# Optimization experiments

Measured on AMD Instinct MI355X. Metric: run time of the kernel, lower is better.

Reference implementation:

```python
import jax, jax.numpy as jnp
import numpy as np

EPS = 1e-6
B, S, D = 2, 2048, 2048
NH, NKV, HD = 16, 4, 128
DFF = 5632
WINDOW = 512


def rmsnorm(x, w):
    var = jnp.mean(x * x, axis=-1, keepdims=True)
    return x * jax.lax.rsqrt(var + EPS) * w


def rotate_half(x):
    x1, x2 = jnp.split(x, 2, axis=-1)
    return jnp.concatenate([-x2, x1], axis=-1)


def apply_rope(x, cos, sin):
    # x: (B, H, S, HD); cos/sin: (S, HD)
    return x * cos[None, None] + rotate_half(x) * sin[None, None]


def setup_inputs() -> dict:
    key = jax.random.key(0)
    ks = jax.random.split(key, 12)
    s = lambda n: (1.0 / np.sqrt(n))
    inp = {
        "hidden_states": jax.random.normal(ks[0], (B, S, D), jnp.float32),
        "cos": jnp.cos(jnp.arange(S)[:, None] / (10000.0 ** (jnp.concatenate([jnp.arange(HD // 2), jnp.arange(HD // 2)]) * 2.0 / HD))),
        "sin": jnp.sin(jnp.arange(S)[:, None] / (10000.0 ** (jnp.concatenate([jnp.arange(HD // 2), jnp.arange(HD // 2)]) * 2.0 / HD))),
        "ln1_w": jnp.ones((D,), jnp.float32),
        "ln2_w": jnp.ones((D,), jnp.float32),
        "wq": jax.random.normal(ks[1], (NH * HD, D), jnp.float32) * s(D),
        "wk": jax.random.normal(ks[2], (NKV * HD, D), jnp.float32) * s(D),
        "wv": jax.random.normal(ks[3], (NKV * HD, D), jnp.float32) * s(D),
        "wo": jax.random.normal(ks[4], (D, NH * HD), jnp.float32) * s(NH * HD),
        "w_gate": jax.random.normal(ks[5], (DFF, D), jnp.float32) * s(D),
        "w_up": jax.random.normal(ks[6], (DFF, D), jnp.float32) * s(D),
        "w_down": jax.random.normal(ks[7], (D, DFF), jnp.float32) * s(DFF),
    }
    return inp


def reference(hidden_states, cos, sin, ln1_w, ln2_w, wq, wk, wv, wo, w_gate, w_up, w_down):
    x = hidden_states
    # --- attention block ---
    h = rmsnorm(x, ln1_w)
    q = jnp.einsum("bsd,ed->bse", h, wq).reshape(B, S, NH, HD).transpose(0, 2, 1, 3)
    k = jnp.einsum("bsd,ed->bse", h, wk).reshape(B, S, NKV, HD).transpose(0, 2, 1, 3)
    v = jnp.einsum("bsd,ed->bse", h, wv).reshape(B, S, NKV, HD).transpose(0, 2, 1, 3)
    q = apply_rope(q, cos, sin)
    k = apply_rope(k, cos, sin)
    rep = NH // NKV
    k = jnp.repeat(k, rep, axis=1)  # (B, NH, S, HD)
    v = jnp.repeat(v, rep, axis=1)
    scale = 1.0 / np.sqrt(HD)
    scores = jnp.einsum("bhqd,bhkd->bhqk", q, k) * scale
    pos = jnp.arange(S)
    diff = pos[:, None] - pos[None, :]
    allowed = (diff >= 0) & (diff < WINDOW)  # causal + sliding window
    scores = jnp.where(allowed[None, None], scores, jnp.finfo(scores.dtype).min)
    attn = jax.nn.softmax(scores, axis=-1)
    out = jnp.einsum("bhqk,bhkd->bhqd", attn, v)
    out = out.transpose(0, 2, 1, 3).reshape(B, S, NH * HD)
    out = jnp.einsum("bse,de->bsd", out, wo)
    x = x + out
    # --- SwiGLU MLP block ---
    h = rmsnorm(x, ln2_w)
    gate = jax.nn.silu(jnp.einsum("bsd,fd->bsf", h, w_gate))
    up = jnp.einsum("bsd,fd->bsf", h, w_up)
    mlp = jnp.einsum("bsf,df->bsd", gate * up, w_down)
    return x + mlp
```

## Files before the change

kernel.cpp:

```cpp
#include <hip/hip_runtime.h>

typedef unsigned short u16;
typedef __attribute__((ext_vector_type(8))) short bf16x8;
typedef __attribute__((ext_vector_type(8))) unsigned short u16x8;
typedef __attribute__((ext_vector_type(4))) float f32x4;
typedef __attribute__((ext_vector_type(4))) _Float16 f16x4;

__device__ __forceinline__ u16 f2bf(float f) {
  union { float f; unsigned u; } v; v.f = f;
  unsigned r = v.u + 0x7fffu + ((v.u >> 16) & 1u);
  return (u16)(r >> 16);
}
__device__ __forceinline__ float bf2f(u16 u) {
  union { unsigned u; float f; } v; v.u = ((unsigned)u) << 16; return v.f;
}

#define GLOBAL_LOAD_LDS16(g, l)                                                \
  __builtin_amdgcn_global_load_lds(                                            \
      (const __attribute__((address_space(1))) void*)(g),                      \
      (__attribute__((address_space(3))) void*)(l), 16, 0, 0)

#define PHASE_SYNC()                                                            \
  __builtin_amdgcn_s_barrier();                                                 \
  asm volatile("s_waitcnt lgkmcnt(0)" ::: "memory");                            \
  __builtin_amdgcn_sched_barrier(0)

__global__ __launch_bounds__(256) void rmsnorm_k(const float* __restrict__ x,
                                                 const float* __restrict__ w,
                                                 u16* __restrict__ out) {
  __shared__ float red[4];
  const int t = threadIdx.x;
  const size_t base = (size_t)blockIdx.x * 2048 + t * 8;
  float4 a = *(const float4*)(x + base);
  float4 b = *(const float4*)(x + base + 4);
  float ss = a.x * a.x + a.y * a.y + a.z * a.z + a.w * a.w +
             b.x * b.x + b.y * b.y + b.z * b.z + b.w * b.w;
#pragma unroll
  for (int o = 32; o; o >>= 1) ss += __shfl_xor(ss, o);
  if ((t & 63) == 0) red[t >> 6] = ss;
  __syncthreads();
  float rs = rsqrtf((red[0] + red[1] + red[2] + red[3]) * (1.0f / 2048.0f) + 1e-6f);
  float4 wa = *(const float4*)(w + t * 8);
  float4 wb = *(const float4*)(w + t * 8 + 4);
  u16x8 o8;
  o8[0] = f2bf(a.x * rs * wa.x); o8[1] = f2bf(a.y * rs * wa.y);
  o8[2] = f2bf(a.z * rs * wa.z); o8[3] = f2bf(a.w * rs * wa.w);
  o8[4] = f2bf(b.x * rs * wb.x); o8[5] = f2bf(b.y * rs * wb.y);
  o8[6] = f2bf(b.z * rs * wb.z); o8[7] = f2bf(b.w * rs * wb.w);
  *(u16x8*)(out + base) = o8;
}

__global__ __launch_bounds__(256) void rope_k(u16* __restrict__ buf,
                                              const float* __restrict__ cosp,
                                              const float* __restrict__ sinp,
                                              int nh, int total) {
  int i = blockIdx.x * 256 + threadIdx.x;
  if (i >= total) return;
  int d = i & 63;
  int hh = (i >> 6) % nh;
  int row = i / (64 * nh);
  int s = row & 2047;
  u16* p = buf + (size_t)row * (nh * 128) + hh * 128 + d;
  float x1 = bf2f(p[0]), x2 = bf2f(p[64]);
  float c1 = cosp[s * 128 + d], s1 = sinp[s * 128 + d];
  float c2 = cosp[s * 128 + d + 64], s2 = sinp[s * 128 + d + 64];
  p[0]  = f2bf(x1 * c1 - x2 * s1);
  p[64] = f2bf(x2 * c2 + x1 * s2);
}

__global__ __launch_bounds__(256) void rope_qkv(u16* __restrict__ buf,
                                                const float* __restrict__ cosp,
                                                const float* __restrict__ sinp) {
  int i = blockIdx.x * 256 + threadIdx.x;
  int d = i & 63;
  int hh = (i >> 6) % 20;
  int row = i / 1280;
  int s = row & 2047;
  int col = (hh < 16) ? hh * 128 + d : 2048 + (hh - 16) * 128 + d;
  u16* p = buf + (size_t)row * 3072 + col;
  float x1 = bf2f(p[0]), x2 = bf2f(p[64]);
  float c1 = cosp[s * 128 + d], s1 = sinp[s * 128 + d];
  float c2 = cosp[s * 128 + d + 64], s2 = sinp[s * 128 + d + 64];
  p[0]  = f2bf(x1 * c1 - x2 * s1);
  p[64] = f2bf(x2 * c2 + x1 * s2);
}

__global__ __launch_bounds__(256) void cvt_k(const float* __restrict__ s,
                                             u16* __restrict__ d, int n) {
  int stride = gridDim.x * 256 * 8;
  for (int i = (blockIdx.x * 256 + threadIdx.x) * 8; i < n; i += stride) {
    float4 a = *(const float4*)(s + i);
    float4 b = *(const float4*)(s + i + 4);
    u16x8 o;
    o[0] = f2bf(a.x); o[1] = f2bf(a.y); o[2] = f2bf(a.z); o[3] = f2bf(a.w);
    o[4] = f2bf(b.x); o[5] = f2bf(b.y); o[6] = f2bf(b.z); o[7] = f2bf(b.w);
    *(u16x8*)(d + i) = o;
  }
}

__global__ __launch_bounds__(256) void cvt3_k(const float* __restrict__ s0,
                                              const float* __restrict__ s1,
                                              const float* __restrict__ s2,
                                              u16* __restrict__ d,
                                              int n0, int n1, int n2) {
  int total = n0 + n1 + n2;
  int stride = gridDim.x * 256 * 8;
  for (int i = (blockIdx.x * 256 + threadIdx.x) * 8; i < total; i += stride) {
    const float* s; int off;
    if (i < n0)            { s = s0; off = i; }
    else if (i < n0 + n1)  { s = s1; off = i - n0; }
    else                   { s = s2; off = i - n0 - n1; }
    float4 a = *(const float4*)(s + off);
    float4 b = *(const float4*)(s + off + 4);
    u16x8 o;
    o[0] = f2bf(a.x); o[1] = f2bf(a.y); o[2] = f2bf(a.z); o[3] = f2bf(a.w);
    o[4] = f2bf(b.x); o[5] = f2bf(b.y); o[6] = f2bf(b.z); o[7] = f2bf(b.w);
    *(u16x8*)(d + i) = o;
  }
}

__device__ __forceinline__ void tile_swz(int bid, int nwg, int tm, int& bm, int& bn) {
  int cpx = nwg >> 3;
  int w = (bid & 7) * cpx + (bid >> 3);
  bm = w % tm;
  bn = w / tm;
}

template <int EPI>
__global__ __launch_bounds__(512, 2) void gemm4p(const u16* __restrict__ A,
                                                 const u16* __restrict__ Bw,
                                                 void* Cout, const float* resid,
                                                 int M, int N, int K) {
  const int NK = K >> 6;
  __shared__ u16 lds[49152];
  const int t = threadIdx.x, lane = t & 63, w = t >> 6;
  const int wm = w >> 2, wn = w & 3;
  const int l15 = lane & 15, lg = lane >> 4;
  int bm, bn;
  tile_swz(blockIdx.x, gridDim.x, M >> 8, bm, bn);

  const int r64 = t >> 3;
  const int gsrc = ((t & 7) ^ (r64 & 7)) * 8;
  const u16* Asrc[4];
#pragma unroll
  for (int u = 0; u < 4; ++u)
    Asrc[u] = A + (size_t)(bm * 256 + u * 64 + r64) * K + gsrc;
  const u16* Bsrc[2];
#pragma unroll
  for (int u = 0; u < 2; ++u)
    Bsrc[u] = Bw + (size_t)(bn * 128 + u * 64 + r64) * K + gsrc;
  const int d0 = t * 8;

#define STG_A4(buf, u, kt)                                                     \
  GLOBAL_LOAD_LDS16(Asrc[u] + (kt) * 64, &lds[(buf) * 24576 + (u) * 4096 + d0])
#define STG_B4(buf, u, kt)                                                     \
  GLOBAL_LOAD_LDS16(Bsrc[u] + (kt) * 64,                                       \
                    &lds[(buf) * 24576 + 16384 + (u) * 4096 + d0])

  const int swz0 = (lg ^ (l15 & 7)) * 8;
  const int swz1 = ((4 + lg) ^ (l15 & 7)) * 8;
  const int abase = (wm * 128 + l15) * 64;
  const int bbase = 16384 + (wn * 32 + l15) * 64;

  f32x4 acc[8][2] = {};
  bf16x8 af[4], bf0[2], bf1[2];

  STG_A4(0, 0, 0); STG_A4(0, 1, 0); STG_A4(0, 2, 0); STG_A4(0, 3, 0);
  STG_B4(0, 0, 0); STG_B4(0, 1, 0);
  STG_B4(1, 0, 1); STG_B4(1, 1, 1);
  asm volatile("s_waitcnt vmcnt(2)" ::: "memory");
  __builtin_amdgcn_s_barrier();

  for (int T = 0; T < NK; ++T) {
    const int bb = (T & 1) * 24576;
    const int nbuf = (T + 1) & 1, cbuf = T & 1;
#pragma unroll
    for (int i = 0; i < 4; ++i)
      af[i] = *(const bf16x8*)&lds[bb + abase + i * 1024 + swz0];
#pragma unroll
    for (int n = 0; n < 2; ++n)
      bf0[n] = *(const bf16x8*)&lds[bb + bbase + n * 1024 + swz0];
    if (T < NK - 1) { STG_A4(nbuf, 0, T + 1); STG_A4(nbuf, 1, T + 1); }
    PHASE_SYNC();
    __builtin_amdgcn_s_setprio(1);
#pragma unroll
    for (int i = 0; i < 4; ++i)
#pragma unroll
      for (int n = 0; n < 2; ++n)
        acc[i][n] = __builtin_amdgcn_mfma_f32_16x16x32_bf16(af[i], bf0[n], acc[i][n], 0, 0, 0);
    __builtin_amdgcn_s_setprio(0);
    __builtin_amdgcn_s_barrier();
#pragma unroll
    for (int i = 0; i < 4; ++i)
      af[i] = *(const bf16x8*)&lds[bb + abase + i * 1024 + swz1];
#pragma unroll
    for (int n = 0; n < 2; ++n)
      bf1[n] = *(const bf16x8*)&lds[bb + bbase + n * 1024 + swz1];
    if (T < NK - 1) { STG_A4(nbuf, 2, T + 1); STG_A4(nbuf, 3, T + 1); }
    PHASE_SYNC();
    __builtin_amdgcn_s_setprio(1);
#pragma unroll
    for (int i = 0; i < 4; ++i)
#pragma unroll
      for (int n = 0; n < 2; ++n)
        acc[i][n] = __builtin_amdgcn_mfma_f32_16x16x32_bf16(af[i], bf1[n], acc[i][n], 0, 0, 0);
    __builtin_amdgcn_s_setprio(0);
    __builtin_amdgcn_s_barrier();
#pragma unroll
    for (int i = 0; i < 4; ++i)
      af[i] = *(const bf16x8*)&lds[bb + abase + (4 + i) * 1024 + swz0];
    if (T < NK - 2) STG_B4(cbuf, 0, T + 2);
    PHASE_SYNC();
    __builtin_amdgcn_s_setprio(1);
#pragma unroll
    for (int i = 0; i < 4; ++i)
#pragma unroll
      for (int n = 0; n < 2; ++n)
        acc[4 + i][n] = __builtin_amdgcn_mfma_f32_16x16x32_bf16(af[i], bf0[n], acc[4 + i][n], 0, 0, 0);
    __builtin_amdgcn_s_setprio(0);
    __builtin_amdgcn_s_barrier();
#pragma unroll
    for (int i = 0; i < 4; ++i)
      af[i] = *(const bf16x8*)&lds[bb + abase + (4 + i) * 1024 + swz1];
    if (T < NK - 2) STG_B4(cbuf, 1, T + 2);
    PHASE_SYNC();
    __builtin_amdgcn_s_setprio(1);
#pragma unroll
    for (int i = 0; i < 4; ++i)
#pragma unroll
      for (int n = 0; n < 2; ++n)
        acc[4 + i][n] = __builtin_amdgcn_mfma_f32_16x16x32_bf16(af[i], bf1[n], acc[4 + i][n], 0, 0, 0);
    __builtin_amdgcn_s_setprio(0);
    if (T < NK - 2) asm volatile("s_waitcnt vmcnt(2)" ::: "memory");
    else            asm volatile("s_waitcnt vmcnt(0)" ::: "memory");
    __builtin_amdgcn_s_barrier();
  }
#undef STG_A4
#undef STG_B4

#pragma unroll
  for (int mf = 0; mf < 8; ++mf)
#pragma unroll
    for (int nf = 0; nf < 2; ++nf)
#pragma unroll
      for (int r = 0; r < 4; ++r) {
        int row = bm * 256 + wm * 128 + mf * 16 + lg * 4 + r;
        int col = bn * 128 + wn * 32 + nf * 16 + l15;
        size_t idx = (size_t)row * N + col;
        if (EPI == 0)
          ((u16*)Cout)[idx] = f2bf(acc[mf][nf][r]);
        else
          ((float*)Cout)[idx] = resid[idx] + acc[mf][nf][r];
      }
}

__global__ __launch_bounds__(512, 2) void gu256(const u16* __restrict__ A,
                                                const u16* __restrict__ Wg,
                                                const u16* __restrict__ Wu,
                                                u16* __restrict__ G) {
  constexpr int KD = 2048, NK = 32;
  __shared__ u16 lds[65536];
  const int t = threadIdx.x, lane = t & 63, w = t >> 6;
  const int wm = w >> 2, wn = w & 3;
  const int l15 = lane & 15, lg = lane >> 4;
  int bm, bn;
  tile_swz(blockIdx.x, gridDim.x, 16, bm, bn);

  const int l8 = lane >> 3, g8 = lane & 7;
  const int gsrc = (g8 ^ l8) * 8;
  const u16* Asrc[2][2];
#pragma unroll
  for (int ha = 0; ha < 2; ++ha)
#pragma unroll
    for (int c = 0; c < 2; ++c)
      Asrc[ha][c] = A + (size_t)(bm * 256 + ha * 128 + w * 16 + c * 8 + l8) * KD + gsrc;
  const u16* Wsel = ((w >> 1) & 1) ? Wu : Wg;
  const u16* Bsrc[2][2];
#pragma unroll
  for (int hb = 0; hb < 2; ++hb)
#pragma unroll
    for (int c = 0; c < 2; ++c)
      Bsrc[hb][c] = Wsel + (size_t)(bn * 128 + (hb * 2 + (w >> 2)) * 32 +
                                    (w & 1) * 16 + c * 8 + l8) * KD + gsrc;
  const int dst_wl = w * 1024 + lane * 8;

#define STG_A(buf, ha, kt) do {                                                \
    GLOBAL_LOAD_LDS16(Asrc[ha][0] + (kt) * 64,                                 \
                      &lds[(buf) * 32768 + (ha) * 8192 + dst_wl]);             \
    GLOBAL_LOAD_LDS16(Asrc[ha][1] + (kt) * 64,                                 \
                      &lds[(buf) * 32768 + (ha) * 8192 + dst_wl + 512]); } while (0)
#define STG_B(buf, hb, kt) do {                                                \
    GLOBAL_LOAD_LDS16(Bsrc[hb][0] + (kt) * 64,                                 \
                      &lds[(buf) * 32768 + 16384 + (hb) * 8192 + dst_wl]);     \
    GLOBAL_LOAD_LDS16(Bsrc[hb][1] + (kt) * 64,                                 \
                      &lds[(buf) * 32768 + 16384 + (hb) * 8192 + dst_wl + 512]); } while (0)

  const int swz0 = (lg ^ (l15 & 7)) * 8;
  const int swz1 = ((4 + lg) ^ (l15 & 7)) * 8;
  const int abase = (wm * 128 + l15) * 64;
  const int bbase = 16384 + (wn * 64 + l15) * 64;

  f32x4 acc[8][4] = {};
  bf16x8 af[4], bf0[4], bf1[4];

  STG_A(0, 0, 0); STG_A(0, 1, 0);
  STG_B(0, 0, 0); STG_B(0, 1, 0);
  STG_B(1, 0, 1); STG_B(1, 1, 1);
  asm volatile("s_waitcnt vmcnt(4)" ::: "memory");
  __builtin_amdgcn_s_barrier();

  for (int T = 0; T < NK; ++T) {
    const int bb = (T & 1) * 32768;
    const int nbuf = (T + 1) & 1, cbuf = T & 1;
#pragma unroll
    for (int i = 0; i < 4; ++i)
      af[i] = *(const bf16x8*)&lds[bb + abase + i * 1024 + swz0];
#pragma unroll
    for (int n = 0; n < 4; ++n)
      bf0[n] = *(const bf16x8*)&lds[bb + bbase + n * 1024 + swz0];
    if (T < NK - 1) STG_A(nbuf, 0, T + 1);
    PHASE_SYNC();
    __builtin_amdgcn_s_setprio(1);
#pragma unroll
    for (int i = 0; i < 4; ++i)
#pragma unroll
      for (int n = 0; n < 4; ++n)
        acc[i][n] = __builtin_amdgcn_mfma_f32_16x16x32_bf16(af[i], bf0[n], acc[i][n], 0, 0, 0);
    __builtin_amdgcn_s_setprio(0);
    __builtin_amdgcn_s_barrier();
#pragma unroll
    for (int i = 0; i < 4; ++i)
      af[i] = *(const bf16x8*)&lds[bb + abase + i * 1024 + swz1];
#pragma unroll
    for (int n = 0; n < 4; ++n)
      bf1[n] = *(const bf16x8*)&lds[bb + bbase + n * 1024 + swz1];
    if (T < NK - 1) STG_A(nbuf, 1, T + 1);
    PHASE_SYNC();
    __builtin_amdgcn_s_setprio(1);
#pragma unroll
    for (int i = 0; i < 4; ++i)
#pragma unroll
      for (int n = 0; n < 4; ++n)
        acc[i][n] = __builtin_amdgcn_mfma_f32_16x16x32_bf16(af[i], bf1[n], acc[i][n], 0, 0, 0);
    __builtin_amdgcn_s_setprio(0);
    __builtin_amdgcn_s_barrier();
#pragma unroll
    for (int i = 0; i < 4; ++i)
      af[i] = *(const bf16x8*)&lds[bb + abase + (4 + i) * 1024 + swz0];
    if (T < NK - 2) STG_B(cbuf, 0, T + 2);
    PHASE_SYNC();
    __builtin_amdgcn_s_setprio(1);
#pragma unroll
    for (int i = 0; i < 4; ++i)
#pragma unroll
      for (int n = 0; n < 4; ++n)
        acc[4 + i][n] = __builtin_amdgcn_mfma_f32_16x16x32_bf16(af[i], bf0[n], acc[4 + i][n], 0, 0, 0);
    __builtin_amdgcn_s_setprio(0);
    __builtin_amdgcn_s_barrier();
#pragma unroll
    for (int i = 0; i < 4; ++i)
      af[i] = *(const bf16x8*)&lds[bb + abase + (4 + i) * 1024 + swz1];
    if (T < NK - 2) STG_B(cbuf, 1, T + 2);
    PHASE_SYNC();
    __builtin_amdgcn_s_setprio(1);
#pragma unroll
    for (int i = 0; i < 4; ++i)
#pragma unroll
      for (int n = 0; n < 4; ++n)
        acc[4 + i][n] = __builtin_amdgcn_mfma_f32_16x16x32_bf16(af[i], bf1[n], acc[4 + i][n], 0, 0, 0);
    __builtin_amdgcn_s_setprio(0);
    if (T < NK - 2) asm volatile("s_waitcnt vmcnt(4)" ::: "memory");
    else            asm volatile("s_waitcnt vmcnt(0)" ::: "memory");
    __builtin_amdgcn_s_barrier();
  }
#undef STG_A
#undef STG_B

  const size_t grow0 = (size_t)(bm * 256 + wm * 128 + lg * 4);
  const int gcol0 = bn * 128 + wn * 32 + l15;
#pragma unroll
  for (int mf = 0; mf < 8; ++mf)
#pragma unroll
    for (int p = 0; p < 2; ++p)
#pragma unroll
      for (int r = 0; r < 4; ++r) {
        float gg = acc[mf][p][r], uu = acc[mf][p + 2][r];
        float sg = gg / (1.0f + __expf(-gg));
        G[(grow0 + mf * 16 + r) * 5632 + gcol0 + p * 16] = f2bf(sg * uu);
      }
}

template <int EPI>
__global__ __launch_bounds__(256) void gemm_bt(const u16* __restrict__ A,
                                               const float* __restrict__ Bw,
                                               void* Cout, const float* resid,
                                               int M, int N, int K) {
  __shared__ u16 sA[128 * 32];
  __shared__ u16 sB[128 * 40];
  const int t = threadIdx.x, lane = t & 63, w = t >> 6;
  const int l15 = lane & 15, lg = lane >> 4;
  const int tn = N >> 7;
  const int bm = blockIdx.x / tn, bn = blockIdx.x % tn;
  const int wr = (w >> 1) << 6, wc = (w & 1) << 6;

  const u16* Ag  = A + (size_t)(bm * 128 + (t >> 2)) * K + (t & 3) * 8;
  const u16* Ag2 = Ag + (size_t)64 * K;
  const float* Bg  = Bw + (size_t)(bn * 128 + (t >> 2)) * K + (t & 3) * 8;
  const float* Bg2 = Bg + (size_t)64 * K;
  u16* sBp  = &sB[(t >> 2) * 40 + (t & 3) * 8];
  u16* sBp2 = sBp + 64 * 40;

  f32x4 acc[4][4] = {};

  for (int kt = 0; kt < K; kt += 32) {
    float4 b0 = *(const float4*)(Bg + kt);
    float4 b1 = *(const float4*)(Bg + kt + 4);
    float4 c0 = *(const float4*)(Bg2 + kt);
    float4 c1 = *(const float4*)(Bg2 + kt + 4);
    GLOBAL_LOAD_LDS16(Ag + kt, &sA[t * 8]);
    GLOBAL_LOAD_LDS16(Ag2 + kt, &sA[64 * 32 + t * 8]);
    u16x8 bs;
    bs[0] = f2bf(b0.x); bs[1] = f2bf(b0.y); bs[2] = f2bf(b0.z); bs[3] = f2bf(b0.w);
    bs[4] = f2bf(b1.x); bs[5] = f2bf(b1.y); bs[6] = f2bf(b1.z); bs[7] = f2bf(b1.w);
    *(u16x8*)sBp = bs;
    bs[0] = f2bf(c0.x); bs[1] = f2bf(c0.y); bs[2] = f2bf(c0.z); bs[3] = f2bf(c0.w);
    bs[4] = f2bf(c1.x); bs[5] = f2bf(c1.y); bs[6] = f2bf(c1.z); bs[7] = f2bf(c1.w);
    *(u16x8*)sBp2 = bs;
    __syncthreads();
    bf16x8 af[4], bfr[4];
#pragma unroll
    for (int m = 0; m < 4; ++m)
      af[m] = *(const bf16x8*)&sA[(wr + m * 16 + l15) * 32 + lg * 8];
#pragma unroll
    for (int n = 0; n < 4; ++n)
      bfr[n] = *(const bf16x8*)&sB[(wc + n * 16 + l15) * 40 + lg * 8];
#pragma unroll
    for (int m = 0; m < 4; ++m)
#pragma unroll
      for (int n = 0; n < 4; ++n)
        acc[m][n] = __builtin_amdgcn_mfma_f32_16x16x32_bf16(af[m], bfr[n], acc[m][n], 0, 0, 0);
    __syncthreads();
  }
#pragma unroll
  for (int m = 0; m < 4; ++m)
#pragma unroll
    for (int n = 0; n < 4; ++n)
#pragma unroll
      for (int r = 0; r < 4; ++r) {
        int row = bm * 128 + wr + m * 16 + lg * 4 + r;
        int col = bn * 128 + wc + n * 16 + l15;
        size_t idx = (size_t)row * N + col;
        if (EPI == 0)
          ((u16*)Cout)[idx] = f2bf(acc[m][n][r]);
        else
          ((float*)Cout)[idx] = resid[idx] + acc[m][n][r];
      }
}

__global__ __launch_bounds__(512) void gemm_gateup(const u16* __restrict__ A,
                                                   const float* __restrict__ Wg,
                                                   const float* __restrict__ Wu,
                                                   u16* __restrict__ G) {
  constexpr int N = 5632, K = 2048;
  __shared__ u16 sA[128 * 32];
  __shared__ u16 sB1[128 * 40];
  __shared__ u16 sB2[128 * 40];
  const int t = threadIdx.x, lane = t & 63, w = t >> 6;
  const int l15 = lane & 15, lg = lane >> 4;
  const int bm = blockIdx.x / 44, bn = blockIdx.x % 44;
  const int wr = (w >> 2) << 6, wc = (w & 3) << 5;

  const u16* Ag = A + (size_t)(bm * 128 + (t >> 2)) * K + (t & 3) * 8;
  const float* Bg1 = Wg + (size_t)(bn * 128 + (t >> 2)) * K + (t & 3) * 8;
  const float* Bg2 = Wu + (size_t)(bn * 128 + (t >> 2)) * K + (t & 3) * 8;
  const int sboff = (t >> 2) * 40 + (t & 3) * 8;

  f32x4 acc1[4][2] = {};
  f32x4 acc2[4][2] = {};

  for (int kt = 0; kt < K; kt += 32) {
    float4 g0 = *(const float4*)(Bg1 + kt);
    float4 g1 = *(const float4*)(Bg1 + kt + 4);
    float4 u0 = *(const float4*)(Bg2 + kt);
    float4 u1 = *(const float4*)(Bg2 + kt + 4);
    GLOBAL_LOAD_LDS16(Ag + kt, &sA[t * 8]);
    u16x8 bs;
    bs[0] = f2bf(g0.x); bs[1] = f2bf(g0.y); bs[2] = f2bf(g0.z); bs[3] = f2bf(g0.w);
    bs[4] = f2bf(g1.x); bs[5] = f2bf(g1.y); bs[6] = f2bf(g1.z); bs[7] = f2bf(g1.w);
    *(u16x8*)&sB1[sboff] = bs;
    bs[0] = f2bf(u0.x); bs[1] = f2bf(u0.y); bs[2] = f2bf(u0.z); bs[3] = f2bf(u0.w);
    bs[4] = f2bf(u1.x); bs[5] = f2bf(u1.y); bs[6] = f2bf(u1.z); bs[7] = f2bf(u1.w);
    *(u16x8*)&sB2[sboff] = bs;
    __syncthreads();
    bf16x8 af[4], b1f[2], b2f[2];
#pragma unroll
    for (int m = 0; m < 4; ++m)
      af[m] = *(const bf16x8*)&sA[(wr + m * 16 + l15) * 32 + lg * 8];
#pragma unroll
    for (int n = 0; n < 2; ++n) {
      b1f[n] = *(const bf16x8*)&sB1[(wc + n * 16 + l15) * 40 + lg * 8];
      b2f[n] = *(const bf16x8*)&sB2[(wc + n * 16 + l15) * 40 + lg * 8];
    }
#pragma unroll
    for (int m = 0; m < 4; ++m)
#pragma unroll
      for (int n = 0; n < 2; ++n) {
        acc1[m][n] = __builtin_amdgcn_mfma_f32_16x16x32_bf16(af[m], b1f[n], acc1[m][n], 0, 0, 0);
        acc2[m][n] = __builtin_amdgcn_mfma_f32_16x16x32_bf16(af[m], b2f[n], acc2[m][n], 0, 0, 0);
      }
    __syncthreads();
  }
#pragma unroll
  for (int m = 0; m < 4; ++m)
#pragma unroll
    for (int n = 0; n < 2; ++n)
#pragma unroll
      for (int r = 0; r < 4; ++r) {
        int row = bm * 128 + wr + m * 16 + lg * 4 + r;
        int col = bn * 128 + wc + n * 16 + l15;
        float ga = acc1[m][n][r], uu = acc2[m][n][r];
        float sg = ga / (1.0f + __expf(-ga));
        G[(size_t)row * N + col] = f2bf(sg * uu);
      }
}

__global__ __launch_bounds__(256) void attn_k(const u16* __restrict__ Q,
                                              const u16* __restrict__ K,
                                              const u16* __restrict__ V,
                                              u16* __restrict__ O,
                                              int qstr, int kvstr) {
  const int lane = threadIdx.x & 63;
  const int wid = blockIdx.x * 4 + (threadIdx.x >> 6);
  const int qt = wid & 127;
  const int h = (wid >> 7) & 15;
  const int b = wid >> 11;
  const int q0 = qt << 4;
  const int kvh = h >> 2;
  const int l15 = lane & 15, lg = lane >> 4;

  bf16x8 qf[4];
  {
    const u16* qp = Q + (size_t)((b << 11) + q0 + l15) * qstr + h * 128 + lg * 8;
#pragma unroll
    for (int ds = 0; ds < 4; ++ds) qf[ds] = *(const bf16x8*)(qp + ds * 32);
  }
  float m_run = -1e30f, l_run = 0.0f;
  f32x4 oacc[8];
#pragma unroll
  for (int db = 0; db < 8; ++db) oacc[db] = f32x4{0.f, 0.f, 0.f, 0.f};

  int lo = q0 - 511;
  if (lo < 0) lo = 0;
  for (int kb = (lo & ~15); kb <= q0; kb += 16) {
    f32x4 st = {0.f, 0.f, 0.f, 0.f};
    const u16* kp = K + (size_t)((b << 11) + kb + l15) * kvstr + kvh * 128 + lg * 8;
#pragma unroll
    for (int ds = 0; ds < 4; ++ds)
      st = __builtin_amdgcn_mfma_f32_16x16x32_bf16(*(const bf16x8*)(kp + ds * 32),
                                                   qf[ds], st, 0, 0, 0);
    const int qpos = q0 + l15;
    float pe[4];
    float tmax = -1e30f;
#pragma unroll
    for (int r = 0; r < 4; ++r) {
      int j = kb + lg * 4 + r;
      int d = qpos - j;
      bool ok = (d >= 0) && (d < 512);
      pe[r] = ok ? st[r] * 0.08838834764831845f : -1e30f;
      tmax = fmaxf(tmax, pe[r]);
    }
    tmax = fmaxf(tmax, __shfl_xor(tmax, 16));
    tmax = fmaxf(tmax, __shfl_xor(tmax, 32));
    float m_new = fmaxf(m_run, tmax);
    float corr = __expf(m_run - m_new);
    float psum = 0.0f;
#pragma unroll
    for (int r = 0; r < 4; ++r) {
      float e = (pe[r] > -1e29f) ? __expf(pe[r] - m_new) : 0.0f;
      pe[r] = e;
      psum += e;
    }
    psum += __shfl_xor(psum, 16);
    psum += __shfl_xor(psum, 32);
    l_run = l_run * corr + psum;
    m_run = m_new;

    f16x4 pf;
#pragma unroll
    for (int r = 0; r < 4; ++r) pf[r] = (_Float16)pe[r];

    float f0 = __shfl(corr, lg * 4 + 0);
    float f1 = __shfl(corr, lg * 4 + 1);
    float f2 = __shfl(corr, lg * 4 + 2);
    float f3 = __shfl(corr, lg * 4 + 3);
    const u16* vp = V + (size_t)((b << 11) + kb + lg * 4) * kvstr + kvh * 128 + l15;
#pragma unroll
    for (int db = 0; db < 8; ++db) {
      oacc[db][0] *= f0; oacc[db][1] *= f1; oacc[db][2] *= f2; oacc[db][3] *= f3;
      f16x4 vf;
#pragma unroll
      for (int e = 0; e < 4; ++e)
        vf[e] = (_Float16)bf2f(vp[(size_t)e * kvstr + db * 16]);
      oacc[db] = __builtin_amdgcn_mfma_f32_16x16x16f16(pf, vf, oacc[db], 0, 0, 0);
    }
  }
  float inv = 1.0f / l_run;
  float g0 = __shfl(inv, lg * 4 + 0);
  float g1 = __shfl(inv, lg * 4 + 1);
  float g2 = __shfl(inv, lg * 4 + 2);
  float g3 = __shfl(inv, lg * 4 + 3);
  u16* op = O + (size_t)((b << 11) + q0 + lg * 4) * 2048 + h * 128 + l15;
#pragma unroll
  for (int db = 0; db < 8; ++db) {
    op[0 * 2048 + db * 16] = f2bf(oacc[db][0] * g0);
    op[1 * 2048 + db * 16] = f2bf(oacc[db][1] * g1);
    op[2 * 2048 + db * 16] = f2bf(oacc[db][2] * g2);
    op[3 * 2048 + db * 16] = f2bf(oacc[db][3] * g3);
  }
}

extern "C" void kernel_launch(void* const* d_in, const int* in_sizes, int n_in,
                              void* d_out, int out_size, void* d_ws, size_t ws_size,
                              hipStream_t stream) {
  const float* x    = (const float*)d_in[0];
  const float* cosp = (const float*)d_in[1];
  const float* sinp = (const float*)d_in[2];
  const float* ln1  = (const float*)d_in[3];
  const float* ln2  = (const float*)d_in[4];
  const float* wq   = (const float*)d_in[5];
  const float* wk   = (const float*)d_in[6];
  const float* wv   = (const float*)d_in[7];
  const float* wo   = (const float*)d_in[8];
  const float* wg   = (const float*)d_in[9];
  const float* wu   = (const float*)d_in[10];
  const float* wd   = (const float*)d_in[11];
  float* out = (float*)d_out;

  const size_t SZ_HQ  = 8388608;
  const size_t SZ_KV  = 2097152;
  const size_t SZ_QKV = 12582912;
  const size_t SZ_G   = 23068672;
  const size_t SZ_WB  = 23068672;
  const size_t need_old = (SZ_HQ * 3 + SZ_KV * 2 + SZ_G) * 2;
  const size_t need_new = (SZ_HQ * 2 + SZ_QKV + SZ_G + SZ_WB) * 2;
  if (ws_size < need_old) return;

  if (ws_size >= need_new) {
    u16* h   = (u16*)d_ws;
    u16* qkv = h + SZ_HQ;
    u16* at  = qkv + SZ_QKV;
    u16* g   = at + SZ_HQ;
    u16* wb  = g + SZ_G;
    u16* wqb = wb;
    u16* wob = wb;
    u16* wgb = wb;
    u16* wdb = wb;

    rmsnorm_k<<<4096, 256, 0, stream>>>(x, ln1, h);
    cvt3_k<<<2048, 256, 0, stream>>>(wq, wk, wv, wqb, 4194304, 1048576, 1048576);
    gemm4p<0><<<384, 512, 0, stream>>>(h, wqb, qkv, nullptr, 4096, 3072, 2048);
    rope_qkv<<<20480, 256, 0, stream>>>(qkv, cosp, sinp);
    attn_k<<<1024, 256, 0, stream>>>(qkv, qkv + 2048, qkv + 2560, at, 3072, 3072);
    cvt_k<<<2048, 256, 0, stream>>>(wo, wob, 4194304);
    gemm4p<1><<<256, 512, 0, stream>>>(at, wob, d_out, x, 4096, 2048, 2048);
    rmsnorm_k<<<4096, 256, 0, stream>>>(out, ln2, h);
    cvt3_k<<<2048, 256, 0, stream>>>(wg, wu, wu, wgb, 11534336, 11534336, 0);
    gu256<<<704, 512, 0, stream>>>(h, wgb, wgb + 11534336, g);
    cvt_k<<<2048, 256, 0, stream>>>(wd, wdb, 11534336);
    gemm4p<1><<<256, 512, 0, stream>>>(g, wdb, d_out, out, 4096, 2048, 5632);
  } else {
    u16* h  = (u16*)d_ws;
    u16* q  = h + SZ_HQ;
    u16* kk = q + SZ_HQ;
    u16* vv = kk + SZ_KV;
    u16* at = vv + SZ_KV;
    u16* g  = at + SZ_HQ;

    rmsnorm_k<<<4096, 256, 0, stream>>>(x, ln1, h);
    gemm_bt<0><<<512, 256, 0, stream>>>(h, wq, q,  nullptr, 4096, 2048, 2048);
    gemm_bt<0><<<128, 256, 0, stream>>>(h, wk, kk, nullptr, 4096, 512, 2048);
    gemm_bt<0><<<128, 256, 0, stream>>>(h, wv, vv, nullptr, 4096, 512, 2048);
    rope_k<<<16384, 256, 0, stream>>>(q, cosp, sinp, 16, 4194304);
    rope_k<<<4096, 256, 0, stream>>>(kk, cosp, sinp, 4, 1048576);
    attn_k<<<1024, 256, 0, stream>>>(q, kk, vv, at, 2048, 512);
    gemm_bt<1><<<512, 256, 0, stream>>>(at, wo, d_out, x, 4096, 2048, 2048);
    rmsnorm_k<<<4096, 256, 0, stream>>>(out, ln2, h);
    gemm_gateup<<<1408, 512, 0, stream>>>(h, wg, wu, g);
    gemm_bt<1><<<512, 256, 0, stream>>>(g, wd, d_out, out, 4096, 2048, 5632);
  }
}
```

Before: 602.8 us.

## Rework GEMM to 128x256 tiles with triple-buffered LDS and fewer barriers

Replaces the 256x128 double-buffered four-phase GEMM with a 128x256 tile kernel that uses a three-stage LDS ring, prefetches two k-tiles ahead and needs one workgroup barrier per k-tile instead of four. The intra-phase barriers are also dropped from the shared phase macro, which affects the gate/up kernel as well. The goal is less barrier stall and deeper load/compute overlap. The cost is more LDS per block (about 147 KB), and the gate/up kernel may now have a write-after-read race on its current buffer without the mid-iteration barriers.

```diff
diff --git a/kernel.cpp b/kernel.cpp
--- a/kernel.cpp
+++ b/kernel.cpp
@@ -20,10 +20,10 @@
       (const __attribute__((address_space(1))) void*)(g),                      \
       (__attribute__((address_space(3))) void*)(l), 16, 0, 0)
 
-#define PHASE_SYNC()                                                            \
-  __builtin_amdgcn_s_barrier();                                                 \
-  asm volatile("s_waitcnt lgkmcnt(0)" ::: "memory");                            \
-  __builtin_amdgcn_sched_barrier(0)
+#define PHASE_TAIL()                                                           \
+  asm volatile("s_waitcnt lgkmcnt(0)" ::: "memory");                           \
+  __builtin_amdgcn_sched_barrier(0);                                           \
+  __builtin_amdgcn_s_setprio(1)
 
 __global__ __launch_bounds__(256) void rmsnorm_k(const float* __restrict__ x,
                                                  const float* __restrict__ w,
@@ -127,125 +127,99 @@
 }
 
 template <int EPI>
-__global__ __launch_bounds__(512, 2) void gemm4p(const u16* __restrict__ A,
+__global__ __launch_bounds__(512, 2) void gemm2p(const u16* __restrict__ A,
                                                  const u16* __restrict__ Bw,
                                                  void* Cout, const float* resid,
                                                  int M, int N, int K) {
   const int NK = K >> 6;
-  __shared__ u16 lds[49152];
+  __shared__ u16 lds[73728];
   const int t = threadIdx.x, lane = t & 63, w = t >> 6;
   const int wm = w >> 2, wn = w & 3;
   const int l15 = lane & 15, lg = lane >> 4;
   int bm, bn;
-  tile_swz(blockIdx.x, gridDim.x, M >> 8, bm, bn);
+  tile_swz(blockIdx.x, gridDim.x, M >> 7, bm, bn);
 
   const int r64 = t >> 3;
   const int gsrc = ((t & 7) ^ (r64 & 7)) * 8;
-  const u16* Asrc[4];
+  const u16* Asrc[2];
+#pragma unroll
+  for (int u = 0; u < 2; ++u)
+    Asrc[u] = A + (size_t)(bm * 128 + u * 64 + r64) * K + gsrc;
+  const u16* Bsrc[4];
 #pragma unroll
   for (int u = 0; u < 4; ++u)
-    Asrc[u] = A + (size_t)(bm * 256 + u * 64 + r64) * K + gsrc;
-  const u16* Bsrc[2];
-#pragma unroll
-  for (int u = 0; u < 2; ++u)
-    Bsrc[u] = Bw + (size_t)(bn * 128 + u * 64 + r64) * K + gsrc;
+    Bsrc[u] = Bw + (size_t)(bn * 256 + u * 64 + r64) * K + gsrc;
   const int d0 = t * 8;
 
-#define STG_A4(buf, u, kt)                                                     \
+#define STG_A2(buf, u, kt)                                                     \
   GLOBAL_LOAD_LDS16(Asrc[u] + (kt) * 64, &lds[(buf) * 24576 + (u) * 4096 + d0])
-#define STG_B4(buf, u, kt)                                                     \
+#define STG_B2(buf, u, kt)                                                     \
   GLOBAL_LOAD_LDS16(Bsrc[u] + (kt) * 64,                                       \
-                    &lds[(buf) * 24576 + 16384 + (u) * 4096 + d0])
+                    &lds[(buf) * 24576 + 8192 + (u) * 4096 + d0])
 
   const int swz0 = (lg ^ (l15 & 7)) * 8;
   const int swz1 = ((4 + lg) ^ (l15 & 7)) * 8;
-  const int abase = (wm * 128 + l15) * 64;
-  const int bbase = 16384 + (wn * 32 + l15) * 64;
-
-  f32x4 acc[8][2] = {};
-  bf16x8 af[4], bf0[2], bf1[2];
-
-  STG_A4(0, 0, 0); STG_A4(0, 1, 0); STG_A4(0, 2, 0); STG_A4(0, 3, 0);
-  STG_B4(0, 0, 0); STG_B4(0, 1, 0);
-  STG_B4(1, 0, 1); STG_B4(1, 1, 1);
-  asm volatile("s_waitcnt vmcnt(2)" ::: "memory");
+  const int abase = wm * 4096 + l15 * 64;
+  const int bbase = 8192 + wn * 4096 + l15 * 64;
+
+  f32x4 acc[4][4] = {};
+  bf16x8 af[4], bfr[4];
+
+  STG_A2(0, 0, 0); STG_A2(0, 1, 0);
+  STG_B2(0, 0, 0); STG_B2(0, 1, 0); STG_B2(0, 2, 0); STG_B2(0, 3, 0);
+  STG_A2(1, 0, 1); STG_A2(1, 1, 1);
+  STG_B2(1, 0, 1); STG_B2(1, 1, 1); STG_B2(1, 2, 1); STG_B2(1, 3, 1);
+  asm volatile("s_waitcnt vmcnt(6)" ::: "memory");
   __builtin_amdgcn_s_barrier();
 
   for (int T = 0; T < NK; ++T) {
-    const int bb = (T & 1) * 24576;
-    const int nbuf = (T + 1) & 1, cbuf = T & 1;
+    const int bb = (T % 3) * 24576;
+    const int nb = (T + 2) % 3;
 #pragma unroll
     for (int i = 0; i < 4; ++i)
       af[i] = *(const bf16x8*)&lds[bb + abase + i * 1024 + swz0];
 #pragma unroll
-    for (int n = 0; n < 2; ++n)
-      bf0[n] = *(const bf16x8*)&lds[bb + bbase + n * 1024 + swz0];
-    if (T < NK - 1) { STG_A4(nbuf, 0, T + 1); STG_A4(nbuf, 1, T + 1); }
-    PHASE_SYNC();
-    __builtin_amdgcn_s_setprio(1);
-#pragma unroll
-    for (int i = 0; i < 4; ++i)
-#pragma unroll
-      for (int n = 0; n < 2; ++n)
-        acc[i][n] = __builtin_amdgcn_mfma_f32_16x16x32_bf16(af[i], bf0[n], acc[i][n], 0, 0, 0);
+    for (int n = 0; n < 4; ++n)
+      bfr[n] = *(const bf16x8*)&lds[bb + bbase + n * 1024 + swz0];
+    if (T < NK - 2) { STG_A2(nb, 0, T + 2); STG_A2(nb, 1, T + 2); STG_B2(nb, 0, T + 2); }
+    PHASE_TAIL();
+#pragma unroll
+    for (int i = 0; i < 4; ++i)
+#pragma unroll
+      for (int n = 0; n < 4; ++n)
+        acc[i][n] = __builtin_amdgcn_mfma_f32_16x16x32_bf16(af[i], bfr[n], acc[i][n], 0, 0, 0);
     __builtin_amdgcn_s_setprio(0);
-    __builtin_amdgcn_s_barrier();
 #pragma unroll
     for (int i = 0; i < 4; ++i)
       af[i] = *(const bf16x8*)&lds[bb + abase + i * 1024 + swz1];
 #pragma unroll
-    for (int n = 0; n < 2; ++n)
-      bf1[n] = *(const bf16x8*)&lds[bb + bbase + n * 1024 + swz1];
-    if (T < NK - 1) { STG_A4(nbuf, 2, T + 1); STG_A4(nbuf, 3, T + 1); }
-    PHASE_SYNC();
-    __builtin_amdgcn_s_setprio(1);
-#pragma unroll
-    for (int i = 0; i < 4; ++i)
-#pragma unroll
-      for (int n = 0; n < 2; ++n)
-        acc[i][n] = __builtin_amdgcn_mfma_f32_16x16x32_bf16(af[i], bf1[n], acc[i][n], 0, 0, 0);
+    for (int n = 0; n < 4; ++n)
+      bfr[n] = *(const bf16x8*)&lds[bb + bbase + n * 1024 + swz1];
+    if (T < NK - 2) { STG_B2(nb, 1, T + 2); STG_B2(nb, 2, T + 2); STG_B2(nb, 3, T + 2); }
+    PHASE_TAIL();
+#pragma unroll
+    for (int i = 0; i < 4; ++i)
+#pragma unroll
+      for (int n = 0; n < 4; ++n)
+        acc[i][n] = __builtin_amdgcn_mfma_f32_16x16x32_bf16(af[i], bfr[n], acc[i][n], 0, 0, 0);
     __builtin_amdgcn_s_setprio(0);
-    __builtin_amdgcn_s_barrier();
-#pragma unroll
-    for (int i = 0; i < 4; ++i)
-      af[i] = *(const bf16x8*)&lds[bb + abase + (4 + i) * 1024 + swz0];
-    if (T < NK - 2) STG_B4(cbuf, 0, T + 2);
-    PHASE_SYNC();
-    __builtin_amdgcn_s_setprio(1);
-#pragma unroll
-    for (int i = 0; i < 4; ++i)
-#pragma unroll
-      for (int n = 0; n < 2; ++n)
-        acc[4 + i][n] = __builtin_amdgcn_mfma_f32_16x16x32_bf16(af[i], bf0[n], acc[4 + i][n], 0, 0, 0);
-    __builtin_amdgcn_s_setprio(0);
-    __builtin_amdgcn_s_barrier();
-#pragma unroll
-    for (int i = 0; i < 4; ++i)
-      af[i] = *(const bf16x8*)&lds[bb + abase + (4 + i) * 1024 + swz1];
-    if (T < NK - 2) STG_B4(cbuf, 1, T + 2);
-    PHASE_SYNC();
-    __builtin_amdgcn_s_setprio(1);
-#pragma unroll
-    for (int i = 0; i < 4; ++i)
-#pragma unroll
-      for (int n = 0; n < 2; ++n)
-        acc[4 + i][n] = __builtin_amdgcn_mfma_f32_16x16x32_bf16(af[i], bf1[n], acc[4 + i][n], 0, 0, 0);
-    __builtin_amdgcn_s_setprio(0);
-    if (T < NK - 2) asm volatile("s_waitcnt vmcnt(2)" ::: "memory");
-    else            asm volatile("s_waitcnt vmcnt(0)" ::: "memory");
-    __builtin_amdgcn_s_barrier();
-  }
-#undef STG_A4
-#undef STG_B4
-
-#pragma unroll
-  for (int mf = 0; mf < 8; ++mf)
-#pragma unroll
-    for (int nf = 0; nf < 2; ++nf)
+    if (T < NK - 1) {
+      if (T < NK - 2) asm volatile("s_waitcnt vmcnt(6)" ::: "memory");
+      else            asm volatile("s_waitcnt vmcnt(0)" ::: "memory");
+      __builtin_amdgcn_s_barrier();
+    }
+  }
+#undef STG_A2
+#undef STG_B2
+
+#pragma unroll
+  for (int mf = 0; mf < 4; ++mf)
+#pragma unroll
+    for (int nf = 0; nf < 4; ++nf)
 #pragma unroll
       for (int r = 0; r < 4; ++r) {
-        int row = bm * 256 + wm * 128 + mf * 16 + lg * 4 + r;
-        int col = bn * 128 + wn * 32 + nf * 16 + l15;
+        int row = bm * 128 + wm * 64 + mf * 16 + lg * 4 + r;
+        int col = bn * 256 + wn * 64 + nf * 16 + l15;
         size_t idx = (size_t)row * N + col;
         if (EPI == 0)
           ((u16*)Cout)[idx] = f2bf(acc[mf][nf][r]);
@@ -319,8 +293,7 @@
     for (int n = 0; n < 4; ++n)
       bf0[n] = *(const bf16x8*)&lds[bb + bbase + n * 1024 + swz0];
     if (T < NK - 1) STG_A(nbuf, 0, T + 1);
-    PHASE_SYNC();
-    __builtin_amdgcn_s_setprio(1);
+    PHASE_TAIL();
 #pragma unroll
     for (int i = 0; i < 4; ++i)
 #pragma unroll
@@ -335,8 +308,7 @@
     for (int n = 0; n < 4; ++n)
       bf1[n] = *(const bf16x8*)&lds[bb + bbase + n * 1024 + swz1];
     if (T < NK - 1) STG_A(nbuf, 1, T + 1);
-    PHASE_SYNC();
-    __builtin_amdgcn_s_setprio(1);
+    PHASE_TAIL();
 #pragma unroll
     for (int i = 0; i < 4; ++i)
 #pragma unroll
@@ -348,8 +320,7 @@
     for (int i = 0; i < 4; ++i)
       af[i] = *(const bf16x8*)&lds[bb + abase + (4 + i) * 1024 + swz0];
     if (T < NK - 2) STG_B(cbuf, 0, T + 2);
-    PHASE_SYNC();
-    __builtin_amdgcn_s_setprio(1);
+    PHASE_TAIL();
 #pragma unroll
     for (int i = 0; i < 4; ++i)
 #pragma unroll
@@ -361,8 +332,7 @@
     for (int i = 0; i < 4; ++i)
       af[i] = *(const bf16x8*)&lds[bb + abase + (4 + i) * 1024 + swz1];
     if (T < NK - 2) STG_B(cbuf, 1, T + 2);
-    PHASE_SYNC();
-    __builtin_amdgcn_s_setprio(1);
+    PHASE_TAIL();
 #pragma unroll
     for (int i = 0; i < 4; ++i)
 #pragma unroll
@@ -658,16 +628,16 @@
 
     rmsnorm_k<<<4096, 256, 0, stream>>>(x, ln1, h);
     cvt3_k<<<2048, 256, 0, stream>>>(wq, wk, wv, wqb, 4194304, 1048576, 1048576);
-    gemm4p<0><<<384, 512, 0, stream>>>(h, wqb, qkv, nullptr, 4096, 3072, 2048);
+    gemm2p<0><<<384, 512, 0, stream>>>(h, wqb, qkv, nullptr, 4096, 3072, 2048);
     rope_qkv<<<20480, 256, 0, stream>>>(qkv, cosp, sinp);
     attn_k<<<1024, 256, 0, stream>>>(qkv, qkv + 2048, qkv + 2560, at, 3072, 3072);
     cvt_k<<<2048, 256, 0, stream>>>(wo, wob, 4194304);
-    gemm4p<1><<<256, 512, 0, stream>>>(at, wob, d_out, x, 4096, 2048, 2048);
+    gemm2p<1><<<256, 512, 0, stream>>>(at, wob, d_out, x, 4096, 2048, 2048);
     rmsnorm_k<<<4096, 256, 0, stream>>>(out, ln2, h);
     cvt3_k<<<2048, 256, 0, stream>>>(wg, wu, wu, wgb, 11534336, 11534336, 0);
     gu256<<<704, 512, 0, stream>>>(h, wgb, wgb + 11534336, g);
     cvt_k<<<2048, 256, 0, stream>>>(wd, wdb, 11534336);
-    gemm4p<1><<<256, 512, 0, stream>>>(g, wdb, d_out, out, 4096, 2048, 5632);
+    gemm2p<1><<<256, 512, 0, stream>>>(g, wdb, d_out, out, 4096, 2048, 5632);
   } else {
     u16* h  = (u16*)d_ws;
     u16* q  = h + SZ_HQ;
```

Result: faster. 570.1 us, median of 3 (-5.4%).
